# Kernel tuning notes

Hardware: AMD Instinct MI355X
Metric: run time of the kernel (lower is better)

The kernel has to match this reference:

```python
import jax, jax.numpy as jnp
from jax import lax
import numpy as np

B, L, C, H, F = 8, 512, 512, 8, 2048
NC, NA, K, W, S = 4, 6, 5, 4, 50
HD = C // H
R = 2 * W + 1
PAD = (K - 1) // 2
H2 = 2
HD2 = C // H2
VOCAB = 256
EPS = 1e-6


def ln_ch(x, g, b):
    # LayerNorm over channel dim of (B,C,L) (torch transposes to (B,L,C), norms last dim)
    m = jnp.mean(x, axis=1, keepdims=True)
    v = jnp.mean((x - m) ** 2, axis=1, keepdims=True)
    return (x - m) * lax.rsqrt(v + EPS) * g[None, :, None] + b[None, :, None]


def conv1x1(w, b, x):
    # 1x1 Conv1d == channel-mixing matmul
    return jnp.einsum('oc,bcl->bol', w, x) + b[None, :, None]


def forward_fn(tokens, style_values, mask, embed,
               cw_dw_w, cw_dw_b, cw_ln_g, cw_ln_b, cw_pw1_w, cw_pw1_b,
               cw_pw2_w, cw_pw2_b, cw_gamma,
               aq_w, aq_b, ak_w, ak_b, av_w, av_b, ao_w, ao_b,
               rel_k_emb, rel_v_emb, ln1_g, ln1_b, ln2_g, ln2_b,
               ffn_w1, ffn_b1, ffn_w2, ffn_b2,
               style_key, sq_w, sq_b, sk_w, sk_b, sv_w, sv_b, so_w, so_b,
               sn_g, sn_b):
    x = embed[tokens]                 # (B,L,C)
    x = jnp.transpose(x, (0, 2, 1))   # (B,C,L)

    # --- ConvNeXt stack ---
    for i in range(NC):
        x = x * mask
        res = x
        xp = jnp.pad(x, ((0, 0), (0, 0), (PAD, PAD)), mode='edge')  # replicate pad
        h = lax.conv_general_dilated(xp, cw_dw_w[i][:, None, :], (1,), 'VALID',
                                     feature_group_count=C,
                                     dimension_numbers=('NCH', 'OIH', 'NCH'))
        h = h + cw_dw_b[i][None, :, None]
        h = h * mask
        h = ln_ch(h, cw_ln_g[i], cw_ln_b[i])
        h = conv1x1(cw_pw1_w[i], cw_pw1_b[i], h)
        h = jax.nn.gelu(h, approximate=False)
        h = conv1x1(cw_pw2_w[i], cw_pw2_b[i], h)
        x = res + cw_gamma[i][None, :, None] * h
        x = x * mask

    # --- AttnEncoder with windowed relative-position attention ---
    x = x * mask
    attn_mask = mask[:, :, :, None] * mask[:, :, None, :]   # (B,1,L,L)
    t = jnp.arange(L)
    diff = t[None, :] - t[:, None]
    wmask = (jnp.abs(diff) <= W).astype(x.dtype)             # (L,L)
    idx = jnp.clip(diff, -W, W) + W                          # (L,L) in [0,2W]
    scale = HD ** -0.5
    for i in range(NA):
        res = x
        q = conv1x1(aq_w[i], aq_b[i], x).reshape(B, H, HD, L).transpose(0, 1, 3, 2) * scale
        k = conv1x1(ak_w[i], ak_b[i], x).reshape(B, H, HD, L).transpose(0, 1, 3, 2)
        v = conv1x1(av_w[i], av_b[i], x).reshape(B, H, HD, L).transpose(0, 1, 3, 2)
        scores = jnp.einsum('bhld,bhmd->bhlm', q, k)
        rel_k = rel_k_emb[i][idx]                             # (L,L,HD)
        scores = scores + jnp.einsum('bhld,lmd->bhlm', q, rel_k) * wmask[None, None]
        scores = jnp.where(attn_mask == 0, -10000.0, scores)
        attn = jax.nn.softmax(scores, axis=-1)
        out = jnp.einsum('bhlm,bhmd->bhld', attn, v)
        rel_v = rel_v_emb[i][idx] * wmask[:, :, None]         # (L,L,HD)
        out = out + jnp.einsum('bhlm,lmd->bhld', attn, rel_v)
        out = out.transpose(0, 1, 3, 2).reshape(B, C, L)
        out = conv1x1(ao_w[i], ao_b[i], out)
        x = ln_ch(res + out, ln1_g[i], ln1_b[i])
        h = conv1x1(ffn_w1[i], ffn_b1[i], x * mask)
        h = jax.nn.relu(h) * mask
        h = conv1x1(ffn_w2[i], ffn_b2[i], h) * mask
        x = ln_ch(x + h, ln2_g[i], ln2_b[i])
    x = x * mask

    # --- StyleAttention ---
    xt = jnp.transpose(x, (0, 2, 1))          # (B,L,C)
    mask_t = jnp.transpose(mask, (0, 2, 1))   # (B,L,1)
    sscale = C ** -0.5                         # torch uses full dim, not head_dim

    def style_layer(xin, i):
        q = (xin @ sq_w[i].T + sq_b[i]).reshape(B, L, H2, HD2)
        kk = jnp.tanh(style_key[0] @ sk_w[i].T + sk_b[i]).reshape(S, H2, HD2)
        vals = jnp.broadcast_to(style_values, (B, S, C))
        vv = (vals @ sv_w[i].T + sv_b[i]).reshape(B, S, H2, HD2)
        sc = jnp.einsum('bthd,shd->hbts', q, kk) * sscale
        a = jax.nn.softmax(sc, axis=-1)
        a = jnp.where(mask_t[None] == 0, 0.0, a)
        o = jnp.einsum('hbts,bshd->bthd', a, vv).reshape(B, L, C)
        o = o @ so_w[i].T + so_b[i]
        return o * mask_t

    out1 = style_layer(xt, 0)
    x1 = xt + out1
    out2 = style_layer(x1, 1)
    x2 = xt + out2
    m = jnp.mean(x2, axis=-1, keepdims=True)
    var = jnp.mean((x2 - m) ** 2, axis=-1, keepdims=True)
    xn = (x2 - m) * lax.rsqrt(var + EPS) * sn_g + sn_b
    x = jnp.transpose(xn, (0, 2, 1)) * mask
    return x


def setup_inputs() -> dict:
    key = jax.random.key(0)
    kit = iter(jax.random.split(key, 48))

    def rn(shape, s=0.02):
        return jax.random.normal(next(kit), shape, jnp.float32) * s

    inp = {
        'tokens': jax.random.randint(next(kit), (B, L), 0, VOCAB),
        'style_values': rn((1, S, C), 1.0),
        'mask': jnp.ones((B, 1, L), jnp.float32),
        'embed': rn((VOCAB, C), 1.0),
        'cw_dw_w': rn((NC, C, K)), 'cw_dw_b': jnp.zeros((NC, C)),
        'cw_ln_g': jnp.ones((NC, C)), 'cw_ln_b': jnp.zeros((NC, C)),
        'cw_pw1_w': rn((NC, 4 * C, C)), 'cw_pw1_b': jnp.zeros((NC, 4 * C)),
        'cw_pw2_w': rn((NC, C, 4 * C)), 'cw_pw2_b': jnp.zeros((NC, C)),
        'cw_gamma': jnp.full((NC, C), 1e-6, jnp.float32),
        'aq_w': rn((NA, C, C)), 'aq_b': jnp.zeros((NA, C)),
        'ak_w': rn((NA, C, C)), 'ak_b': jnp.zeros((NA, C)),
        'av_w': rn((NA, C, C)), 'av_b': jnp.zeros((NA, C)),
        'ao_w': rn((NA, C, C)), 'ao_b': jnp.zeros((NA, C)),
        'rel_k_emb': rn((NA, R, HD)), 'rel_v_emb': rn((NA, R, HD)),
        'ln1_g': jnp.ones((NA, C)), 'ln1_b': jnp.zeros((NA, C)),
        'ln2_g': jnp.ones((NA, C)), 'ln2_b': jnp.zeros((NA, C)),
        'ffn_w1': rn((NA, F, C)), 'ffn_b1': jnp.zeros((NA, F)),
        'ffn_w2': rn((NA, C, F)), 'ffn_b2': jnp.zeros((NA, C)),
        'style_key': rn((1, S, C)),
        'sq_w': rn((2, C, C)), 'sq_b': jnp.zeros((2, C)),
        'sk_w': rn((2, C, C)), 'sk_b': jnp.zeros((2, C)),
        'sv_w': rn((2, C, C)), 'sv_b': jnp.zeros((2, C)),
        'so_w': rn((2, C, C)), 'so_b': jnp.zeros((2, C)),
        'sn_g': jnp.ones((C,)), 'sn_b': jnp.zeros((C,)),
    }
    return inp


def reference(tokens, style_values, mask, embed,
              cw_dw_w, cw_dw_b, cw_ln_g, cw_ln_b, cw_pw1_w, cw_pw1_b,
              cw_pw2_w, cw_pw2_b, cw_gamma,
              aq_w, aq_b, ak_w, ak_b, av_w, av_b, ao_w, ao_b,
              rel_k_emb, rel_v_emb, ln1_g, ln1_b, ln2_g, ln2_b,
              ffn_w1, ffn_b1, ffn_w2, ffn_b2,
              style_key, sq_w, sq_b, sk_w, sk_b, sv_w, sv_b, so_w, so_b,
              sn_g, sn_b):
    return forward_fn(tokens, style_values, mask, embed,
                      cw_dw_w, cw_dw_b, cw_ln_g, cw_ln_b, cw_pw1_w, cw_pw1_b,
                      cw_pw2_w, cw_pw2_b, cw_gamma,
                      aq_w, aq_b, ak_w, ak_b, av_w, av_b, ao_w, ao_b,
                      rel_k_emb, rel_v_emb, ln1_g, ln1_b, ln2_g, ln2_b,
                      ffn_w1, ffn_b1, ffn_w2, ffn_b2,
                      style_key, sq_w, sq_b, sk_w, sk_b, sv_w, sv_b, so_w, so_b,
                      sn_g, sn_b)
```

## Files before the change

### kernel.cpp

```cpp
#include <hip/hip_runtime.h>
#include <cstdint>

#define Bb 8
#define Ll 512
#define Cc 512
#define Hh 8
#define HD 64
#define Ff 2048
#define Ss 50
#define NROWS 4096
#define QKVS 1536

typedef __attribute__((ext_vector_type(8))) short short8v;
typedef __attribute__((ext_vector_type(4))) float f32x4;

__device__ __forceinline__ float wave_sum(float v){
  #pragma unroll
  for (int o=32;o>=1;o>>=1) v += __shfl_xor(v,o);
  return v;
}
__device__ __forceinline__ float bf2f(unsigned short u){
  return __uint_as_float(((unsigned)u) << 16);
}

// ... 377 lines not shown
    if (s+1 < nsteps){
      int ko = (s+1) << 5;
      ah_ = *(const short8v*)(Ahg + ko);
      al_ = *(const short8v*)(Alg + ko);
      bh0_ = *(const short8v*)(Bhg + ko);
      bl0_ = *(const short8v*)(Blg + ko);
      if constexpr (NF==4){
        bh1_ = *(const short8v*)(Bhg + (size_t)64*K + ko);
        bl1_ = *(const short8v*)(Blg + (size_t)64*K + ko);
      }
      if (AMASK && am == 0.f){ ah_ ^= ah_; al_ ^= al_; }
    }
    __syncthreads();
    int fr = lane & 15, fc = (lane >> 4) << 3;
    short8v ahf[2], alf[2], bhf[NF], blf[NF];
    #pragma unroll
    for (int mt=0; mt<2; ++mt){
      int r = (wr<<5) + (mt<<4) + fr;
      ahf[mt] = *(const short8v*)&AhS[st][r][fc];
      alf[mt] = *(const short8v*)&AlS[st][r][fc];
    }
    #pragma unroll
    for (int nt=0; nt<NF; ++nt){
      int r = (NF==4 ? (wc<<6) : (wc<<5)) + (nt<<4) + fr;
      bhf[nt] = *(const short8v*)&BhS[st][r][fc];
      blf[nt] = *(const short8v*)&BlS[st][r][fc];
    }
    #pragma unroll
    for (int mt=0; mt<2; ++mt)
      #pragma unroll
      for (int nt=0; nt<NF; ++nt){
        f32x4 c = acc[mt][nt];
        c = __builtin_amdgcn_mfma_f32_16x16x32_bf16(ahf[mt], bhf[nt], c, 0,0,0);
        c = __builtin_amdgcn_mfma_f32_16x16x32_bf16(ahf[mt], blf[nt], c, 0,0,0);
        c = __builtin_amdgcn_mfma_f32_16x16x32_bf16(alf[mt], bhf[nt], c, 0,0,0);
        acc[mt][nt] = c;
      }
    if (s+1 < nsteps){
      int nb = st ^ 1;
      *(short8v*)&AhS[nb][sr][sc] = ah_;
      *(short8v*)&AlS[nb][sr][sc] = al_;
      *(short8v*)&BhS[nb][sr][sc] = bh0_;
      *(short8v*)&BlS[nb][sr][sc] = bl0_;
      if constexpr (NF==4){
        *(short8v*)&BhS[nb][sr+64][sc] = bh1_;
        *(short8v*)&BlS[nb][sr+64][sc] = bl1_;
      }
    }
    st ^= 1;
  }

  int rb = row0 + (wr<<5) + ((lane>>4)<<2);
  int cb = col0 + (NF==4 ? (wc<<6) : (wc<<5)) + (lane & 15);
  float bs[NF], gm[NF];
  int which = 0;
  if constexpr (EPI==EPI_QKV) which = blockIdx.x >> 2;
  #pragma unroll
  for (int nt=0; nt<NF; ++nt){
    int col = cb + (nt<<4);
    if constexpr (EPI==EPI_QKV){
      const float* bp = (which==0) ? bias : (which==1) ? res : gamma;
      bs[nt] = bp[col & 511];
    } else {
      bs[nt] = bias[col];
      if constexpr (EPI==EPI_RES_GAMMA_MASK) gm[nt] = gamma[col];
    }
  }
  float qscale = 1.f;
  if constexpr (EPI==EPI_QKV) qscale = (which==0) ? scale : 1.f;

  if constexpr (OUT==2){
    if (which == 2){
      #pragma unroll
      for (int mt=0; mt<2; ++mt){
        int row = rb + (mt<<4);
        int b = row >> 9, tok = row & 511;
        #pragma unroll
        for (int nt=0; nt<NF; ++nt){
          int dglob = cb + (nt<<4) - 1024;
          size_t vt = ((size_t)b*512 + dglob)*512 + tok;
          unsigned short h4[4], l4[4];
          #pragma unroll
          for (int j=0; j<4; ++j)
            splitc(acc[mt][nt][j] + bs[nt], h4[j], l4[j]);
          *(ushort4*)&VTh[vt] = make_ushort4(h4[0],h4[1],h4[2],h4[3]);
          *(ushort4*)&VTl[vt] = make_ushort4(l4[0],l4[1],l4[2],l4[3]);
        }
      }
      return;
    }
    #pragma unroll
    for (int mt=0; mt<2; ++mt)
      #pragma unroll
      for (int j=0; j<4; ++j){
        int row = rb + (mt<<4) + j;
        #pragma unroll
        for (int nt=0; nt<NF; ++nt){
          float v = (acc[mt][nt][j] + bs[nt]) * qscale;
          size_t oidx = (size_t)row*O + cb + (nt<<4);
          unsigned short h,l; splitc(v,h,l); Yh[oidx]=h; Yl[oidx]=l;
        }
      }
    return;
  }

  #pragma unroll
  for (int mt=0; mt<2; ++mt)
    #pragma unroll
    for (int j=0; j<4; ++j){
      int row = rb + (mt<<4) + j;
      float rm = 1.f;
      if constexpr (EPI==EPI_RELU_MASK || EPI==EPI_RES_MASK || EPI==EPI_RES_GAMMA_MASK)
        rm = rowmask[row];
      const float* rr = nullptr;
      if constexpr (EPI==EPI_RES || EPI==EPI_RES_MASK || EPI==EPI_RES_GAMMA_MASK)
        rr = res + (size_t)row*O + cb;
      #pragma unroll
      for (int nt=0; nt<NF; ++nt){
        float v = acc[mt][nt][j] + bs[nt];
        if constexpr (EPI==EPI_SCALE) v *= scale;
        else if constexpr (EPI==EPI_QKV) v *= qscale;
        else if constexpr (EPI==EPI_GELU) v = 0.5f*v*(1.f+erff(v*0.7071067811865475f));
        else if constexpr (EPI==EPI_RES) v = rr[nt<<4] + v;
        else if constexpr (EPI==EPI_RELU_MASK) v = fmaxf(v,0.f)*rm;
        else if constexpr (EPI==EPI_RES_MASK) v = rr[nt<<4] + v*rm;
        else if constexpr (EPI==EPI_RES_GAMMA_MASK) v = (rr[nt<<4] + gm[nt]*v)*rm;
        size_t oidx = (size_t)row*O + cb + (nt<<4);
        if constexpr (OUT==0) Y[oidx] = v;
        else if constexpr (OUT==3){
          Y[oidx] = v;
          unsigned short h,l; splitc(v,h,l); Yh[oidx]=h; Yl[oidx]=l;
        }
        else { unsigned short h,l; splitc(v,h,l); Yh[oidx]=h; Yl[oidx]=l; }
      }
    }
}

template<int EPI, bool AMASK, int OUT>
__global__ __launch_bounds__(256) void gemm_big(
    const unsigned short* __restrict__ Ah, const unsigned short* __restrict__ Al,
    const unsigned short* __restrict__ Wh, const unsigned short* __restrict__ Wl,
    const float* __restrict__ bias, const float* __restrict__ res,
    const float* __restrict__ gamma, const float* __restrict__ rowmask,
    float* __restrict__ Y, unsigned short* __restrict__ Yh,
    unsigned short* __restrict__ Yl, unsigned short* __restrict__ VTh,
    unsigned short* __restrict__ VTl, int K, int O, float scale)
{
  __shared__ unsigned short AhS[128][40], AlS[128][40];
  __shared__ unsigned short BhS[128][40], BlS[128][40];
  int t = threadIdx.x;
  int row0 = blockIdx.y << 7, col0 = blockIdx.x << 7;
  int lane = t & 63, wid = t >> 6;
  int wr = wid >> 1, wc = wid & 1;

  int sr = t >> 2, sc = (t & 3) << 3;
  const unsigned short* Ahg = Ah + (size_t)(row0 + sr)*K + sc;
  const unsigned short* Alg = Al + (size_t)(row0 + sr)*K + sc;
  const unsigned short* Bhg = Wh + (size_t)(col0 + sr)*K + sc;
  const unsigned short* Blg = Wl + (size_t)(col0 + sr)*K + sc;
  bool az0 = false, az1 = false;
  if (AMASK){ az0 = (rowmask[row0+sr] == 0.f); az1 = (rowmask[row0+sr+64] == 0.f); }

  f32x4 acc[4][4] = {};
  int nsteps = K >> 5;
  short8v a0h,a0l,a1h,a1l,b0h,b0l,b1h,b1l;
  a0h = *(const short8v*)(Ahg);
  a0l = *(const short8v*)(Alg);
  a1h = *(const short8v*)(Ahg + (size_t)64*K);
  a1l = *(const short8v*)(Alg + (size_t)64*K);
  b0h = *(const short8v*)(Bhg);
  b0l = *(const short8v*)(Blg);
  b1h = *(const short8v*)(Bhg + (size_t)64*K);
  b1l = *(const short8v*)(Blg + (size_t)64*K);

  for (int s = 0; s < nsteps; ++s){
    if (AMASK){
      if (az0){ a0h ^= a0h; a0l ^= a0l; }
      if (az1){ a1h ^= a1h; a1l ^= a1l; }
    }
    __syncthreads();
    *(short8v*)&AhS[sr][sc] = a0h;    *(short8v*)&AlS[sr][sc] = a0l;
    *(short8v*)&AhS[sr+64][sc] = a1h; *(short8v*)&AlS[sr+64][sc] = a1l;
    *(short8v*)&BhS[sr][sc] = b0h;    *(short8v*)&BlS[sr][sc] = b0l;
    *(short8v*)&BhS[sr+64][sc] = b1h; *(short8v*)&BlS[sr+64][sc] = b1l;
    __syncthreads();
    if (s+1 < nsteps){
      int ko = (s+1) << 5;
      a0h = *(const short8v*)(Ahg + ko);
      a0l = *(const short8v*)(Alg + ko);
      a1h = *(const short8v*)(Ahg + (size_t)64*K + ko);
      a1l = *(const short8v*)(Alg + (size_t)64*K + ko);
      b0h = *(const short8v*)(Bhg + ko);
      b0l = *(const short8v*)(Blg + ko);
      b1h = *(const short8v*)(Bhg + (size_t)64*K + ko);
      b1l = *(const short8v*)(Blg + (size_t)64*K + ko);
    }
    int fr = lane & 15, fc = (lane >> 4) << 3;
    short8v ahf[4], alf[4], bhf[4], blf[4];
    #pragma unroll
    for (int mt=0; mt<4; ++mt){
      int r = (wr<<6) + (mt<<4) + fr;
      ahf[mt] = *(const short8v*)&AhS[r][fc];
      alf[mt] = *(const short8v*)&AlS[r][fc];
    }
    #pragma unroll
    for (int nt=0; nt<4; ++nt){
      int r = (wc<<6) + (nt<<4) + fr;
      bhf[nt] = *(const short8v*)&BhS[r][fc];
      blf[nt] = *(const short8v*)&BlS[r][fc];
    }
    #pragma unroll
    for (int mt=0; mt<4; ++mt)
      #pragma unroll
      for (int nt=0; nt<4; ++nt){
        f32x4 c = acc[mt][nt];
        c = __builtin_amdgcn_mfma_f32_16x16x32_bf16(ahf[mt], bhf[nt], c, 0,0,0);
        c = __builtin_amdgcn_mfma_f32_16x16x32_bf16(ahf[mt], blf[nt], c, 0,0,0);
        c = __builtin_amdgcn_mfma_f32_16x16x32_bf16(alf[mt], bhf[nt], c, 0,0,0);
        acc[mt][nt] = c;
      }
  }

  int rb = row0 + (wr<<6) + ((lane>>4)<<2);
  int cb = col0 + (wc<<6) + (lane & 15);
  float bs[4];
  int which = 0;
  if constexpr (EPI==EPI_QKV) which = blockIdx.x >> 2;
  #pragma unroll
  for (int nt=0; nt<4; ++nt){
    int col = cb + (nt<<4);
    if constexpr (EPI==EPI_QKV){
      const float* bp = (which==0) ? bias : (which==1) ? res : gamma;
      bs[nt] = bp[col & 511];
    } else {
      bs[nt] = bias[col];
    }
  }
  float qscale = 1.f;
  if constexpr (EPI==EPI_QKV) qscale = (which==0) ? scale : 1.f;

  if constexpr (OUT==2){
    if (which == 2){
      #pragma unroll
      for (int mt=0; mt<4; ++mt){
        int row = rb + (mt<<4);
        int b = row >> 9, tok = row & 511;
        #pragma unroll
        for (int nt=0; nt<4; ++nt){
          int dglob = cb + (nt<<4) - 1024;
          size_t vt = ((size_t)b*512 + dglob)*512 + tok;
          unsigned short h4[4], l4[4];
          #pragma unroll
          for (int j=0; j<4; ++j)
            splitc(acc[mt][nt][j] + bs[nt], h4[j], l4[j]);
          *(ushort4*)&VTh[vt] = make_ushort4(h4[0],h4[1],h4[2],h4[3]);
          *(ushort4*)&VTl[vt] = make_ushort4(l4[0],l4[1],l4[2],l4[3]);
        }
      }
      return;
    }
    #pragma unroll
    for (int mt=0; mt<4; ++mt)
      #pragma unroll
      for (int j=0; j<4; ++j){
        int row = rb + (mt<<4) + j;
        #pragma unroll
        for (int nt=0; nt<4; ++nt){
          float v = (acc[mt][nt][j] + bs[nt]) * qscale;
          size_t oidx = (size_t)row*O + cb + (nt<<4);
          unsigned short h,l; splitc(v,h,l); Yh[oidx]=h; Yl[oidx]=l;
        }
      }
    return;
  }

  #pragma unroll
  for (int mt=0; mt<4; ++mt)
    #pragma unroll
    for (int j=0; j<4; ++j){
      int row = rb + (mt<<4) + j;
      float rm = 1.f;
      if constexpr (EPI==EPI_RELU_MASK) rm = rowmask[row];
      #pragma unroll
      for (int nt=0; nt<4; ++nt){
        float v = acc[mt][nt][j] + bs[nt];
        if constexpr (EPI==EPI_GELU) v = 0.5f*v*(1.f+erff(v*0.7071067811865475f));
        else if constexpr (EPI==EPI_RELU_MASK) v = fmaxf(v,0.f)*rm;
        size_t oidx = (size_t)row*O + cb + (nt<<4);
        if constexpr (OUT==0) Y[oidx] = v;
        else { unsigned short h,l; splitc(v,h,l); Yh[oidx]=h; Yl[oidx]=l; }
      }
    }
}

__global__ __launch_bounds__(256) void attn_mf(
    const unsigned short* __restrict__ Ph_g, const unsigned short* __restrict__ Pl_g,
    const unsigned short* __restrict__ VTh_g, const unsigned short* __restrict__ VTl_g,
    const float* __restrict__ relk, const float* __restrict__ relv,
    const float* __restrict__ mask, unsigned short* __restrict__ Oh,
    unsigned short* __restrict__ Ol)
{
  __shared__ float ms_[512];
  __shared__ float rv[9][64];
  __shared__ float qrel[16][16];
  __shared__ float red1[4][16];
  __shared__ float red2[4][16];
  __shared__ __align__(16) unsigned short Spool[16*520];
  unsigned short (*Qh)[72]  = (unsigned short(*)[72])(Spool);
  unsigned short (*Ql)[72]  = (unsigned short(*)[72])(Spool + 1152);
  unsigned short (*Rkh)[72] = (unsigned short(*)[72])(Spool + 2304);
  unsigned short (*Rkl)[72] = (unsigned short(*)[72])(Spool + 3456);
  unsigned short (*Sp)[520] = (unsigned short(*)[520])(Spool);

  int id = blockIdx.x;
  int xcd = id & 7, kk = id >> 3;
  int bh_ = xcd*8 + (kk >> 5);
  int qt = kk & 31;
  int h = bh_ & 7, b_ = bh_ >> 3;
  int t = threadIdx.x;
  int l0 = qt * 16;
  const size_t rowoff = (size_t)b_ * 512;
  int lane = t & 63, w = t >> 6;

  ms_[t] = mask[rowoff + t]; ms_[t+256] = mask[rowoff + t + 256];
  for (int i = t; i < 576; i += 256) ((float*)rv)[i] = relv[i];
  {
    int r = t >> 4, c = (t & 15) << 2;
    float4 v;
    if (r < 9) v = *(const float4*)&relk[r*64 + c];
    else { v.x=0.f; v.y=0.f; v.z=0.f; v.w=0.f; }
    split4(v, &Rkh[r][c], &Rkl[r][c]);
  }
  {
    int idx = t & 127; int r = idx >> 3, c = (idx & 7) << 3;
    size_t g = (rowoff + l0 + r)*QKVS + h*64 + c;
    if (t < 128) *(short8v*)&Qh[r][c] = *(const short8v*)&Ph_g[g];
    else         *(short8v*)&Ql[r][c] = *(const short8v*)&Pl_g[g];
  }
  __syncthreads();

  int fr = lane & 15, fc = (lane >> 4) << 3;
  int qbase = (lane>>4) << 2;
  short8v ah0 = *(const short8v*)&Qh[fr][fc];
  short8v ah1 = *(const short8v*)&Qh[fr][32+fc];
  short8v al0 = *(const short8v*)&Ql[fr][fc];
  short8v al1 = *(const short8v*)&Ql[fr][32+fc];

  if (w == 0){
    short8v rh0 = *(const short8v*)&Rkh[fr][fc];
    short8v rh1 = *(const short8v*)&Rkh[fr][32+fc];
    short8v rl0 = *(const short8v*)&Rkl[fr][fc];
    short8v rl1 = *(const short8v*)&Rkl[fr][32+fc];
    f32x4 c4 = {};
    c4 = __builtin_amdgcn_mfma_f32_16x16x32_bf16(ah0,rh0,c4,0,0,0);
    c4 = __builtin_amdgcn_mfma_f32_16x16x32_bf16(ah1,rh1,c4,0,0,0);
    c4 = __builtin_amdgcn_mfma_f32_16x16x32_bf16(ah0,rl0,c4,0,0,0);
    c4 = __builtin_amdgcn_mfma_f32_16x16x32_bf16(ah1,rl1,c4,0,0,0);
    c4 = __builtin_amdgcn_mfma_f32_16x16x32_bf16(al0,rh0,c4,0,0,0);
    c4 = __builtin_amdgcn_mfma_f32_16x16x32_bf16(al1,rh1,c4,0,0,0);
    #pragma unroll
    for (int j = 0; j < 4; ++j) qrel[qbase + j][fr] = c4[j];
  }
  __syncthreads();

  f32x4 sreg[8];
  #pragma unroll
  for (int tt = 0; tt < 8; ++tt){
    int br = tt*64 + w*16 + fr;
    const unsigned short* krh = Ph_g + (rowoff + br)*QKVS + 512 + h*64;
    const unsigned short* krl = Pl_g + (rowoff + br)*QKVS + 512 + h*64;
    short8v bh0 = *(const short8v*)(krh + fc);
    short8v bh1 = *(const short8v*)(krh + 32 + fc);
    short8v bl0 = *(const short8v*)(krl + fc);
    short8v bl1 = *(const short8v*)(krl + 32 + fc);
    f32x4 c4 = {};
    c4 = __builtin_amdgcn_mfma_f32_16x16x32_bf16(ah0,bh0,c4,0,0,0);
    c4 = __builtin_amdgcn_mfma_f32_16x16x32_bf16(ah1,bh1,c4,0,0,0);
    c4 = __builtin_amdgcn_mfma_f32_16x16x32_bf16(ah0,bl0,c4,0,0,0);
    c4 = __builtin_amdgcn_mfma_f32_16x16x32_bf16(ah1,bl1,c4,0,0,0);
    c4 = __builtin_amdgcn_mfma_f32_16x16x32_bf16(al0,bh0,c4,0,0,0);
    c4 = __builtin_amdgcn_mfma_f32_16x16x32_bf16(al1,bh1,c4,0,0,0);
    int m = tt*64 + w*16 + fr;
    float mm_ = ms_[m];
    #pragma unroll
    for (int j = 0; j < 4; ++j){
      int q = qbase + j;
      int l = l0 + q;
      float s = c4[j];
      int dlt = m - l + 4;
      if (dlt >= 0 && dlt <= 8) s += qrel[q][dlt];
      if (ms_[l] * mm_ == 0.f) s = -10000.f;
      c4[j] = s;
    }
    sreg[tt] = c4;
  }

  float mx[4], sm[4], inv[4];
  #pragma unroll
  for (int j = 0; j < 4; ++j){
    float v = sreg[0][j];
    #pragma unroll
    for (int tt = 1; tt < 8; ++tt) v = fmaxf(v, sreg[tt][j]);
    #pragma unroll
    for (int o = 8; o >= 1; o >>= 1) v = fmaxf(v, __shfl_xor(v, o));
    mx[j] = v;
  }
  if (fr == 0){
    #pragma unroll
    for (int j = 0; j < 4; ++j) red1[w][qbase + j] = mx[j];
  }
  __syncthreads();
  #pragma unroll
  for (int j = 0; j < 4; ++j){
    int q = qbase + j;
    mx[j] = fmaxf(fmaxf(red1[0][q], red1[1][q]), fmaxf(red1[2][q], red1[3][q]));
  }
  #pragma unroll
  for (int j = 0; j < 4; ++j) sm[j] = 0.f;
  #pragma unroll
  for (int tt = 0; tt < 8; ++tt){
    f32x4 c4 = sreg[tt];
    #pragma unroll
    for (int j = 0; j < 4; ++j){
      float e = expf(c4[j] - mx[j]);
      c4[j] = e;
      sm[j] += e;
    }
    sreg[tt] = c4;
  }
  #pragma unroll
  for (int j = 0; j < 4; ++j){
    float v = sm[j];
    #pragma unroll
    for (int o = 8; o >= 1; o >>= 1) v += __shfl_xor(v, o);
    sm[j] = v;
  }
  if (fr == 0){
    #pragma unroll
    for (int j = 0; j < 4; ++j) red2[w][qbase + j] = sm[j];
  }
  #pragma unroll
  for (int tt = 0; tt < 8; ++tt){
    int m = tt*64 + w*16 + fr;
    #pragma unroll
    for (int j = 0; j < 4; ++j)
      Sp[qbase + j][m] = f2bf_rne(sreg[tt][j]);
  }
  __syncthreads();
  #pragma unroll
  for (int j = 0; j < 4; ++j){
    int q = qbase + j;
    inv[j] = 1.f / (red2[0][q] + red2[1][q] + red2[2][q] + red2[3][q]);
  }

  f32x4 oacc = {};
  const unsigned short* vrh = VTh_g + ((size_t)b_*512 + h*64 + w*16 + fr)*512;
  const unsigned short* vrl = VTl_g + ((size_t)b_*512 + h*64 + w*16 + fr)*512;
  #pragma unroll
  for (int tt = 0; tt < 8; ++tt){
    #pragma unroll
    for (int ks = 0; ks < 2; ++ks){
      int moff = tt*64 + ks*32 + fc;
      short8v ap = *(const short8v*)&Sp[fr][moff];
      short8v bh = *(const short8v*)(vrh + moff);
      short8v bl = *(const short8v*)(vrl + moff);
      oacc = __builtin_amdgcn_mfma_f32_16x16x32_bf16(ap,bh,oacc,0,0,0);
      oacc = __builtin_amdgcn_mfma_f32_16x16x32_bf16(ap,bl,oacc,0,0,0);
    }
  }
  {
    int d = w*16 + fr;
    #pragma unroll
    for (int j = 0; j < 4; ++j){
      int q = qbase + j;
      int l = l0 + q;
      float val = oacc[j];
      #pragma unroll
      for (int dlt = 0; dlt < 9; ++dlt){
        int m = l + dlt - 4;
        if (m >= 0 && m < 512){
          float e = bf2f(Sp[q][m]);
          val += e * rv[dlt][d];
        }
      }
      val *= inv[j];
      unsigned short hh, ll_; splitc(val, hh, ll_);
      size_t oidx = ((rowoff + l) << 9) + h*64 + d;
      Oh[oidx] = hh; Ol[oidx] = ll_;
    }
  }
}

__global__ __launch_bounds__(256) void transpose_out_k(const float* __restrict__ xn,
    const float* __restrict__ mask, float* __restrict__ out){
  __shared__ float tile[32][33];
  int b_ = blockIdx.z; int c0 = blockIdx.x*32; int l0 = blockIdx.y*32;
  int tx = threadIdx.x & 31, ty = threadIdx.x >> 5;
  #pragma unroll
  for (int r=0;r<4;r++){
    int l = l0 + ty + r*8;
    tile[ty + r*8][tx] = xn[(((size_t)(b_*512 + l))<<9) + c0 + tx];
  }
  __syncthreads();
  float mm = mask[b_*512 + l0 + tx];
  #pragma unroll
  for (int r=0;r<4;r++){
    int c = c0 + ty + r*8;
    out[(((size_t)(b_*512 + c))<<9) + l0 + tx] = tile[tx][ty + r*8] * mm;
  }
}

extern "C" void kernel_launch(void* const* d_in, const int* in_sizes, int n_in,
                              void* d_out, int out_size, void* d_ws, size_t ws_size,
                              hipStream_t stream) {
  const int*   tokens   = (const int*)  d_in[0];
  const float* style_v  = (const float*)d_in[1];
  const float* mask     = (const float*)d_in[2];
  const float* embed_w  = (const float*)d_in[3];
  const float* cw_dw_w  = (const float*)d_in[4];
  const float* cw_dw_b  = (const float*)d_in[5];
  const float* cw_ln_g  = (const float*)d_in[6];
  const float* cw_ln_b  = (const float*)d_in[7];
  const float* cw_pw1_w = (const float*)d_in[8];
  const float* cw_pw1_b = (const float*)d_in[9];
  const float* cw_pw2_w = (const float*)d_in[10];
  const float* cw_pw2_b = (const float*)d_in[11];
  const float* cw_gamma = (const float*)d_in[12];
  const float* aq_w = (const float*)d_in[13];
  const float* aq_b = (const float*)d_in[14];
  const float* ak_w = (const float*)d_in[15];
  const float* ak_b = (const float*)d_in[16];
  const float* av_w = (const float*)d_in[17];
  const float* av_b = (const float*)d_in[18];
  const float* ao_w = (const float*)d_in[19];
  const float* ao_b = (const float*)d_in[20];
  const float* rel_k = (const float*)d_in[21];
  const float* rel_v = (const float*)d_in[22];
  const float* ln1_g = (const float*)d_in[23];
  const float* ln1_b = (const float*)d_in[24];
  const float* ln2_g = (const float*)d_in[25];
  const float* ln2_b = (const float*)d_in[26];
  const float* ffn_w1 = (const float*)d_in[27];
  const float* ffn_b1 = (const float*)d_in[28];
  const float* ffn_w2 = (const float*)d_in[29];
  const float* ffn_b2 = (const float*)d_in[30];
  const float* style_key = (const float*)d_in[31];
  const float* sq_w = (const float*)d_in[32];
  const float* sq_b = (const float*)d_in[33];
  const float* sk_w = (const float*)d_in[34];
  const float* sk_b = (const float*)d_in[35];
  const float* sv_w = (const float*)d_in[36];
  const float* sv_b = (const float*)d_in[37];
  const float* so_w = (const float*)d_in[38];
  const float* so_b = (const float*)d_in[39];
  const float* sn_g = (const float*)d_in[40];
  const float* sn_b = (const float*)d_in[41];

  const int N = NROWS;
  char* cur = (char*)d_ws;
  auto nextF = [&](size_t n)->float*{ float* p=(float*)cur; cur += n*sizeof(float); return p; };
  auto nextU = [&](size_t n)->unsigned short*{ unsigned short* p=(unsigned short*)cur; cur += n*2; return p; };

  float* X   = nextF((size_t)N*512);
  float* T   = nextF((size_t)N*512);
  float* Qb  = nextF((size_t)N*512);
  float* Vb  = nextF((size_t)N*512);
  unsigned short* Xh = nextU((size_t)N*512);
  unsigned short* Xl = nextU((size_t)N*512);
  unsigned short* Th = nextU((size_t)N*512);
  unsigned short* Tl = nextU((size_t)N*512);
  unsigned short* Hbh = nextU((size_t)N*2048);
  unsigned short* Hbl = nextU((size_t)N*2048);
  unsigned short* QKVh = nextU((size_t)N*QKVS);
  unsigned short* QKVl = nextU((size_t)N*QKVS);
  unsigned short* VTh = nextU((size_t)8*512*512);
  unsigned short* VTl = nextU((size_t)8*512*512);
  unsigned short* pw1h = nextU(4194304); unsigned short* pw1l = nextU(4194304);
  unsigned short* pw2h = nextU(4194304); unsigned short* pw2l = nextU(4194304);
  unsigned short* qkvh = nextU((size_t)6*QKVS*512); unsigned short* qkvl = nextU((size_t)6*QKVS*512);
  unsigned short* aoh  = nextU(1572864); unsigned short* aol  = nextU(1572864);
  unsigned short* f1h  = nextU(6291456); unsigned short* f1l  = nextU(6291456);
  unsigned short* f2h  = nextU(6291456); unsigned short* f2l  = nextU(6291456);
  unsigned short* sqh  = nextU(524288);  unsigned short* sql  = nextU(524288);
  unsigned short* soh  = nextU(524288);  unsigned short* sol  = nextU(524288);
  unsigned short* KKsh = nextU(65536); unsigned short* KKsl = nextU(65536);
  unsigned short* VTsh = nextU(65536); unsigned short* VTsl = nextU(65536);

  split_all<<<dim3(512,8),256,0,stream>>>(cw_pw1_w, cw_pw2_w, ao_w, ffn_w1,
      ffn_w2, sq_w, so_w, aq_w, ak_w, av_w,
      pw1h, pw1l, pw2h, pw2l, aoh, aol, f1h, f1l, f2h, f2l,
      sqh, sql, soh, sol, qkvh, qkvl);

  dim3 gm512(8,64), gbig2048(16,32), gbigqkv(12,32);

  embed_k<<<4096,128,0,stream>>>(tokens, embed_w, mask, X);

  for (int i=0;i<4;i++){
    dwln_k<<<4096,128,0,stream>>>(X, cw_dw_w + (size_t)i*512*5, cw_dw_b + i*512,
        mask, cw_ln_g+i*512, cw_ln_b+i*512, Th, Tl);
    gemm_big<EPI_GELU,false,1><<<gbig2048,256,0,stream>>>(Th, Tl,
        pw1h + (size_t)i*1048576, pw1l + (size_t)i*1048576,
        cw_pw1_b+i*2048, nullptr, nullptr, nullptr, nullptr, Hbh, Hbl,
        nullptr, nullptr, 512, 2048, 0.f);
    if (i < 3)
      gemm_ps<EPI_RES_GAMMA_MASK,false,0,2><<<gm512,256,0,stream>>>(Hbh, Hbl,
          pw2h + (size_t)i*1048576, pw2l + (size_t)i*1048576,
          cw_pw2_b+i*512, X, cw_gamma+i*512, mask, X, nullptr, nullptr,
          nullptr, nullptr, 2048, 512, 0.f);
    else
      gemm_ps<EPI_RES_GAMMA_MASK,false,3,2><<<gm512,256,0,stream>>>(Hbh, Hbl,
          pw2h + (size_t)i*1048576, pw2l + (size_t)i*1048576,
          cw_pw2_b+i*512, X, cw_gamma+i*512, mask, X, Xh, Xl,
          nullptr, nullptr, 2048, 512, 0.f);
  }

  for (int i=0;i<6;i++){
    gemm_big<EPI_QKV,false,2><<<gbigqkv,256,0,stream>>>(Xh, Xl,
        qkvh + (size_t)i*QKVS*512, qkvl + (size_t)i*QKVS*512,
        aq_b+i*512, ak_b+i*512, av_b+i*512, nullptr, nullptr, QKVh, QKVl,
        VTh, VTl, 512, QKVS, 0.125f);
    attn_mf<<<2048,256,0,stream>>>(QKVh, QKVl, VTh, VTl,
        rel_k + (size_t)i*9*64, rel_v + (size_t)i*9*64, mask, Th, Tl);
    gemm_ps<EPI_RES,false,0,2><<<gm512,256,0,stream>>>(Th, Tl,
        aoh + (size_t)i*262144, aol + (size_t)i*262144,
        ao_b+i*512, X, nullptr, nullptr, Qb, nullptr, nullptr,
        nullptr, nullptr, 512, 512, 0.f);
    ln_rows<true,false><<<1024,256,0,stream>>>(Qb, ln1_g+i*512, ln1_b+i*512,
        nullptr, X, Xh, Xl, N);
    gemm_big<EPI_RELU_MASK,true,1><<<gbig2048,256,0,stream>>>(Xh, Xl,
        f1h + (size_t)i*1048576, f1l + (size_t)i*1048576,
        ffn_b1+i*2048, nullptr, nullptr, mask, nullptr, Hbh, Hbl,
        nullptr, nullptr, 512, 2048, 0.f);
    gemm_ps<EPI_RES_MASK,false,0,2><<<gm512,256,0,stream>>>(Hbh, Hbl,
        f2h + (size_t)i*1048576, f2l + (size_t)i*1048576,
        ffn_b2+i*512, X, nullptr, mask, Qb, nullptr, nullptr,
        nullptr, nullptr, 2048, 512, 0.f);
    if (i < 5)
      ln_rows<true,false><<<1024,256,0,stream>>>(Qb, ln2_g+i*512, ln2_b+i*512,
          nullptr, X, Xh, Xl, N);
    else
      ln_rows<true,true><<<1024,256,0,stream>>>(Qb, ln2_g+i*512, ln2_b+i*512,
          mask, X, Xh, Xl, N);
  }

  style_prep<<<dim3(8,4),256,0,stream>>>(style_key, style_v, sk_w, sk_b,
      sv_w, sv_b, KKsh, KKsl, VTsh, VTsl);

  gemm_ps<EPI_BIAS,false,1,2><<<gm512,256,0,stream>>>(Xh, Xl, sqh, sql,
      sq_b, nullptr, nullptr, nullptr, nullptr, QKVh, QKVl,
      nullptr, nullptr, 512, 512, 0.f);
  style_mf<<<256,256,0,stream>>>(QKVh, QKVl, KKsh, KKsl, VTsh, VTsl,
      mask, Th, Tl);
  gemm_ps<EPI_RES_MASK,false,1,2><<<gm512,256,0,stream>>>(Th, Tl, soh, sol,
      so_b, X, nullptr, mask, nullptr, Hbh, Hbl,
      nullptr, nullptr, 512, 512, 0.f);
  gemm_ps<EPI_BIAS,false,1,2><<<gm512,256,0,stream>>>(Hbh, Hbl, sqh+262144, sql+262144,
      sq_b+512, nullptr, nullptr, nullptr, nullptr, QKVh, QKVl,
      nullptr, nullptr, 512, 512, 0.f);
  style_mf<<<256,256,0,stream>>>(QKVh, QKVl, KKsh+32768, KKsl+32768,
      VTsh+32768, VTsl+32768, mask, Th, Tl);
  gemm_ps<EPI_RES_MASK,false,0,2><<<gm512,256,0,stream>>>(Th, Tl, soh+262144, sol+262144,
      so_b+512, X, nullptr, mask, Vb, nullptr, nullptr,
      nullptr, nullptr, 512, 512, 0.f);

  ln_rows<false,false><<<1024,256,0,stream>>>(Vb, sn_g, sn_b, nullptr,
      Qb, nullptr, nullptr, N);
  transpose_out_k<<<dim3(16,16,8),256,0,stream>>>(Qb, mask, (float*)d_out);
}
```

Measured before the change: 1.804 ms.

## Process 32 query rows per attention block to reuse K and V loads

The attention kernel now handles two 16-row query tiles per block, so each wave's K and V fragments loaded from global memory feed two MFMA accumulators instead of one. The grid shrinks from 2048 to 1024 blocks and the shared-memory buffers double in size. This halves the redundant K/V global traffic per query. In exchange it raises register pressure (two sets of score registers) and LDS use, which may lower occupancy.

```diff
diff --git a/kernel.cpp b/kernel.cpp
--- a/kernel.cpp
+++ b/kernel.cpp
@@ -703,23 +703,23 @@
 {
   __shared__ float ms_[512];
   __shared__ float rv[9][64];
-  __shared__ float qrel[16][16];
-  __shared__ float red1[4][16];
-  __shared__ float red2[4][16];
-  __shared__ __align__(16) unsigned short Spool[16*520];
+  __shared__ float qrel[32][16];
+  __shared__ float red1[4][32];
+  __shared__ float red2[4][32];
+  __shared__ __align__(16) unsigned short Spool[32*520];
   unsigned short (*Qh)[72]  = (unsigned short(*)[72])(Spool);
-  unsigned short (*Ql)[72]  = (unsigned short(*)[72])(Spool + 1152);
-  unsigned short (*Rkh)[72] = (unsigned short(*)[72])(Spool + 2304);
-  unsigned short (*Rkl)[72] = (unsigned short(*)[72])(Spool + 3456);
+  unsigned short (*Ql)[72]  = (unsigned short(*)[72])(Spool + 2304);
+  unsigned short (*Rkh)[72] = (unsigned short(*)[72])(Spool + 4608);
+  unsigned short (*Rkl)[72] = (unsigned short(*)[72])(Spool + 5760);
   unsigned short (*Sp)[520] = (unsigned short(*)[520])(Spool);
 
   int id = blockIdx.x;
   int xcd = id & 7, kk = id >> 3;
-  int bh_ = xcd*8 + (kk >> 5);
-  int qt = kk & 31;
+  int bh_ = xcd*8 + (kk >> 4);
+  int qt = kk & 15;
   int h = bh_ & 7, b_ = bh_ >> 3;
   int t = threadIdx.x;
-  int l0 = qt * 16;
+  int l0 = qt * 32;
   const size_t rowoff = (size_t)b_ * 512;
   int lane = t & 63, w = t >> 6;
 
@@ -732,39 +732,47 @@
     else { v.x=0.f; v.y=0.f; v.z=0.f; v.w=0.f; }
     split4(v, &Rkh[r][c], &Rkl[r][c]);
   }
-  {
-    int idx = t & 127; int r = idx >> 3, c = (idx & 7) << 3;
+  for (int i = t; i < 512; i += 256){
+    int r = (i & 255) >> 3, c = (i & 7) << 3;
     size_t g = (rowoff + l0 + r)*QKVS + h*64 + c;
-    if (t < 128) *(short8v*)&Qh[r][c] = *(const short8v*)&Ph_g[g];
+    if (i < 256) *(short8v*)&Qh[r][c] = *(const short8v*)&Ph_g[g];
     else         *(short8v*)&Ql[r][c] = *(const short8v*)&Pl_g[g];
   }
   __syncthreads();
 
   int fr = lane & 15, fc = (lane >> 4) << 3;
   int qbase = (lane>>4) << 2;
-  short8v ah0 = *(const short8v*)&Qh[fr][fc];
-  short8v ah1 = *(const short8v*)&Qh[fr][32+fc];
-  short8v al0 = *(const short8v*)&Ql[fr][fc];
-  short8v al1 = *(const short8v*)&Ql[fr][32+fc];
-
-  if (w == 0){
+  short8v a0h0 = *(const short8v*)&Qh[fr][fc];
+  short8v a0h1 = *(const short8v*)&Qh[fr][32+fc];
+  short8v a0l0 = *(const short8v*)&Ql[fr][fc];
+  short8v a0l1 = *(const short8v*)&Ql[fr][32+fc];
+  short8v a1h0 = *(const short8v*)&Qh[16+fr][fc];
+  short8v a1h1 = *(const short8v*)&Qh[16+fr][32+fc];
+  short8v a1l0 = *(const short8v*)&Ql[16+fr][fc];
+  short8v a1l1 = *(const short8v*)&Ql[16+fr][32+fc];
+
+  if (w < 2){
     short8v rh0 = *(const short8v*)&Rkh[fr][fc];
     short8v rh1 = *(const short8v*)&Rkh[fr][32+fc];
     short8v rl0 = *(const short8v*)&Rkl[fr][fc];
     short8v rl1 = *(const short8v*)&Rkl[fr][32+fc];
+    short8v qa0 = (w==0) ? a0h0 : a1h0;
+    short8v qa1 = (w==0) ? a0h1 : a1h1;
+    short8v qb0 = (w==0) ? a0l0 : a1l0;
+    short8v qb1 = (w==0) ? a0l1 : a1l1;
     f32x4 c4 = {};
-    c4 = __builtin_amdgcn_mfma_f32_16x16x32_bf16(ah0,rh0,c4,0,0,0);
-    c4 = __builtin_amdgcn_mfma_f32_16x16x32_bf16(ah1,rh1,c4,0,0,0);
-    c4 = __builtin_amdgcn_mfma_f32_16x16x32_bf16(ah0,rl0,c4,0,0,0);
-    c4 = __builtin_amdgcn_mfma_f32_16x16x32_bf16(ah1,rl1,c4,0,0,0);
-    c4 = __builtin_amdgcn_mfma_f32_16x16x32_bf16(al0,rh0,c4,0,0,0);
-    c4 = __builtin_amdgcn_mfma_f32_16x16x32_bf16(al1,rh1,c4,0,0,0);
-    #pragma unroll
-    for (int j = 0; j < 4; ++j) qrel[qbase + j][fr] = c4[j];
+    c4 = __builtin_amdgcn_mfma_f32_16x16x32_bf16(qa0,rh0,c4,0,0,0);
+    c4 = __builtin_amdgcn_mfma_f32_16x16x32_bf16(qa1,rh1,c4,0,0,0);
+    c4 = __builtin_amdgcn_mfma_f32_16x16x32_bf16(qa0,rl0,c4,0,0,0);
+    c4 = __builtin_amdgcn_mfma_f32_16x16x32_bf16(qa1,rl1,c4,0,0,0);
+    c4 = __builtin_amdgcn_mfma_f32_16x16x32_bf16(qb0,rh0,c4,0,0,0);
+    c4 = __builtin_amdgcn_mfma_f32_16x16x32_bf16(qb1,rh1,c4,0,0,0);
+    #pragma unroll
+    for (int j = 0; j < 4; ++j) qrel[w*16 + qbase + j][fr] = c4[j];
   }
   __syncthreads();
 
-  f32x4 sreg[8];
+  f32x4 sreg0[8], sreg1[8];
   #pragma unroll
   for (int tt = 0; tt < 8; ++tt){
     int br = tt*64 + w*16 + fr;
@@ -774,87 +782,123 @@
     short8v bh1 = *(const short8v*)(krh + 32 + fc);
     short8v bl0 = *(const short8v*)(krl + fc);
     short8v bl1 = *(const short8v*)(krl + 32 + fc);
-    f32x4 c4 = {};
-    c4 = __builtin_amdgcn_mfma_f32_16x16x32_bf16(ah0,bh0,c4,0,0,0);
-    c4 = __builtin_amdgcn_mfma_f32_16x16x32_bf16(ah1,bh1,c4,0,0,0);
-    c4 = __builtin_amdgcn_mfma_f32_16x16x32_bf16(ah0,bl0,c4,0,0,0);
-    c4 = __builtin_amdgcn_mfma_f32_16x16x32_bf16(ah1,bl1,c4,0,0,0);
-    c4 = __builtin_amdgcn_mfma_f32_16x16x32_bf16(al0,bh0,c4,0,0,0);
-    c4 = __builtin_amdgcn_mfma_f32_16x16x32_bf16(al1,bh1,c4,0,0,0);
+    f32x4 c0 = {}, c1 = {};
+    c0 = __builtin_amdgcn_mfma_f32_16x16x32_bf16(a0h0,bh0,c0,0,0,0);
+    c1 = __builtin_amdgcn_mfma_f32_16x16x32_bf16(a1h0,bh0,c1,0,0,0);
+    c0 = __builtin_amdgcn_mfma_f32_16x16x32_bf16(a0h1,bh1,c0,0,0,0);
+    c1 = __builtin_amdgcn_mfma_f32_16x16x32_bf16(a1h1,bh1,c1,0,0,0);
+    c0 = __builtin_amdgcn_mfma_f32_16x16x32_bf16(a0h0,bl0,c0,0,0,0);
+    c1 = __builtin_amdgcn_mfma_f32_16x16x32_bf16(a1h0,bl0,c1,0,0,0);
+    c0 = __builtin_amdgcn_mfma_f32_16x16x32_bf16(a0h1,bl1,c0,0,0,0);
+    c1 = __builtin_amdgcn_mfma_f32_16x16x32_bf16(a1h1,bl1,c1,0,0,0);
+    c0 = __builtin_amdgcn_mfma_f32_16x16x32_bf16(a0l0,bh0,c0,0,0,0);
+    c1 = __builtin_amdgcn_mfma_f32_16x16x32_bf16(a1l0,bh0,c1,0,0,0);
+    c0 = __builtin_amdgcn_mfma_f32_16x16x32_bf16(a0l1,bh1,c0,0,0,0);
+    c1 = __builtin_amdgcn_mfma_f32_16x16x32_bf16(a1l1,bh1,c1,0,0,0);
     int m = tt*64 + w*16 + fr;
     float mm_ = ms_[m];
     #pragma unroll
     for (int j = 0; j < 4; ++j){
       int q = qbase + j;
-      int l = l0 + q;
-      float s = c4[j];
-      int dlt = m - l + 4;
-      if (dlt >= 0 && dlt <= 8) s += qrel[q][dlt];
-      if (ms_[l] * mm_ == 0.f) s = -10000.f;
-      c4[j] = s;
-    }
-    sreg[tt] = c4;
-  }
-
-  float mx[4], sm[4], inv[4];
+      {
+        int l = l0 + q;
+        float s = c0[j];
+        int dlt = m - l + 4;
+        if (dlt >= 0 && dlt <= 8) s += qrel[q][dlt];
+        if (ms_[l] * mm_ == 0.f) s = -10000.f;
+        c0[j] = s;
+      }
+      {
+        int l = l0 + 16 + q;
+        float s = c1[j];
+        int dlt = m - l + 4;
+        if (dlt >= 0 && dlt <= 8) s += qrel[16 + q][dlt];
+        if (ms_[l] * mm_ == 0.f) s = -10000.f;
+        c1[j] = s;
+      }
+    }
+    sreg0[tt] = c0; sreg1[tt] = c1;
+  }
+
+  float mx0[4], mx1[4], sm0[4], sm1[4], inv0[4], inv1[4];
   #pragma unroll
   for (int j = 0; j < 4; ++j){
-    float v = sreg[0][j];
-    #pragma unroll
-    for (int tt = 1; tt < 8; ++tt) v = fmaxf(v, sreg[tt][j]);
-    #pragma unroll
-    for (int o = 8; o >= 1; o >>= 1) v = fmaxf(v, __shfl_xor(v, o));
-    mx[j] = v;
+    float v0 = sreg0[0][j], v1 = sreg1[0][j];
+    #pragma unroll
+    for (int tt = 1; tt < 8; ++tt){
+      v0 = fmaxf(v0, sreg0[tt][j]);
+      v1 = fmaxf(v1, sreg1[tt][j]);
+    }
+    #pragma unroll
+    for (int o = 8; o >= 1; o >>= 1){
+      v0 = fmaxf(v0, __shfl_xor(v0, o));
+      v1 = fmaxf(v1, __shfl_xor(v1, o));
+    }
+    mx0[j] = v0; mx1[j] = v1;
   }
   if (fr == 0){
     #pragma unroll
-    for (int j = 0; j < 4; ++j) red1[w][qbase + j] = mx[j];
+    for (int j = 0; j < 4; ++j){
+      red1[w][qbase + j] = mx0[j];
+      red1[w][16 + qbase + j] = mx1[j];
+    }
   }
   __syncthreads();
   #pragma unroll
   for (int j = 0; j < 4; ++j){
     int q = qbase + j;
-    mx[j] = fmaxf(fmaxf(red1[0][q], red1[1][q]), fmaxf(red1[2][q], red1[3][q]));
-  }
-  #pragma unroll
-  for (int j = 0; j < 4; ++j) sm[j] = 0.f;
+    mx0[j] = fmaxf(fmaxf(red1[0][q], red1[1][q]), fmaxf(red1[2][q], red1[3][q]));
+    mx1[j] = fmaxf(fmaxf(red1[0][16+q], red1[1][16+q]), fmaxf(red1[2][16+q], red1[3][16+q]));
+  }
+  #pragma unroll
+  for (int j = 0; j < 4; ++j){ sm0[j] = 0.f; sm1[j] = 0.f; }
   #pragma unroll
   for (int tt = 0; tt < 8; ++tt){
-    f32x4 c4 = sreg[tt];
+    f32x4 c0 = sreg0[tt], c1 = sreg1[tt];
     #pragma unroll
     for (int j = 0; j < 4; ++j){
-      float e = expf(c4[j] - mx[j]);
-      c4[j] = e;
-      sm[j] += e;
-    }
-    sreg[tt] = c4;
+      float e0 = expf(c0[j] - mx0[j]);
+      float e1 = expf(c1[j] - mx1[j]);
+      c0[j] = e0; c1[j] = e1;
+      sm0[j] += e0; sm1[j] += e1;
+    }
+    sreg0[tt] = c0; sreg1[tt] = c1;
   }
   #pragma unroll
   for (int j = 0; j < 4; ++j){
-    float v = sm[j];
-    #pragma unroll
-    for (int o = 8; o >= 1; o >>= 1) v += __shfl_xor(v, o);
-    sm[j] = v;
+    float v0 = sm0[j], v1 = sm1[j];
+    #pragma unroll
+    for (int o = 8; o >= 1; o >>= 1){
+      v0 += __shfl_xor(v0, o);
+      v1 += __shfl_xor(v1, o);
+    }
+    sm0[j] = v0; sm1[j] = v1;
   }
   if (fr == 0){
     #pragma unroll
-    for (int j = 0; j < 4; ++j) red2[w][qbase + j] = sm[j];
+    for (int j = 0; j < 4; ++j){
+      red2[w][qbase + j] = sm0[j];
+      red2[w][16 + qbase + j] = sm1[j];
+    }
   }
   #pragma unroll
   for (int tt = 0; tt < 8; ++tt){
     int m = tt*64 + w*16 + fr;
     #pragma unroll
-    for (int j = 0; j < 4; ++j)
-      Sp[qbase + j][m] = f2bf_rne(sreg[tt][j]);
+    for (int j = 0; j < 4; ++j){
+      Sp[qbase + j][m]      = f2bf_rne(sreg0[tt][j]);
+      Sp[16 + qbase + j][m] = f2bf_rne(sreg1[tt][j]);
+    }
   }
   __syncthreads();
   #pragma unroll
   for (int j = 0; j < 4; ++j){
     int q = qbase + j;
-    inv[j] = 1.f / (red2[0][q] + red2[1][q] + red2[2][q] + red2[3][q]);
-  }
-
-  f32x4 oacc = {};
+    inv0[j] = 1.f / (red2[0][q] + red2[1][q] + red2[2][q] + red2[3][q]);
+    inv1[j] = 1.f / (red2[0][16+q] + red2[1][16+q] + red2[2][16+q] + red2[3][16+q]);
+  }
+
+  f32x4 oacc0 = {}, oacc1 = {};
   const unsigned short* vrh = VTh_g + ((size_t)b_*512 + h*64 + w*16 + fr)*512;
   const unsigned short* vrl = VTl_g + ((size_t)b_*512 + h*64 + w*16 + fr)*512;
   #pragma unroll
@@ -862,32 +906,54 @@
     #pragma unroll
     for (int ks = 0; ks < 2; ++ks){
       int moff = tt*64 + ks*32 + fc;
-      short8v ap = *(const short8v*)&Sp[fr][moff];
+      short8v ap0 = *(const short8v*)&Sp[fr][moff];
+      short8v ap1 = *(const short8v*)&Sp[16+fr][moff];
       short8v bh = *(const short8v*)(vrh + moff);
       short8v bl = *(const short8v*)(vrl + moff);
-      oacc = __builtin_amdgcn_mfma_f32_16x16x32_bf16(ap,bh,oacc,0,0,0);
-      oacc = __builtin_amdgcn_mfma_f32_16x16x32_bf16(ap,bl,oacc,0,0,0);
+      oacc0 = __builtin_amdgcn_mfma_f32_16x16x32_bf16(ap0,bh,oacc0,0,0,0);
+      oacc1 = __builtin_amdgcn_mfma_f32_16x16x32_bf16(ap1,bh,oacc1,0,0,0);
+      oacc0 = __builtin_amdgcn_mfma_f32_16x16x32_bf16(ap0,bl,oacc0,0,0,0);
+      oacc1 = __builtin_amdgcn_mfma_f32_16x16x32_bf16(ap1,bl,oacc1,0,0,0);
     }
   }
   {
     int d = w*16 + fr;
     #pragma unroll
     for (int j = 0; j < 4; ++j){
-      int q = qbase + j;
-      int l = l0 + q;
-      float val = oacc[j];
-      #pragma unroll
-      for (int dlt = 0; dlt < 9; ++dlt){
-        int m = l + dlt - 4;
-        if (m >= 0 && m < 512){
-          float e = bf2f(Sp[q][m]);
-          val += e * rv[dlt][d];
+      {
+        int q = qbase + j;
+        int l = l0 + q;
+        float val = oacc0[j];
+        #pragma unroll
+        for (int dlt = 0; dlt < 9; ++dlt){
+          int m = l + dlt - 4;
+          if (m >= 0 && m < 512){
+            float e = bf2f(Sp[q][m]);
+            val += e * rv[dlt][d];
+          }
         }
-      }
-      val *= inv[j];
-      unsigned short hh, ll_; splitc(val, hh, ll_);
-      size_t oidx = ((rowoff + l) << 9) + h*64 + d;
-      Oh[oidx] = hh; Ol[oidx] = ll_;
+        val *= inv0[j];
+        unsigned short hh, ll_; splitc(val, hh, ll_);
+        size_t oidx = ((rowoff + l) << 9) + h*64 + d;
+        Oh[oidx] = hh; Ol[oidx] = ll_;
+      }
+      {
+        int q = 16 + qbase + j;
+        int l = l0 + q;
+        float val = oacc1[j];
+        #pragma unroll
+        for (int dlt = 0; dlt < 9; ++dlt){
+          int m = l + dlt - 4;
+          if (m >= 0 && m < 512){
+            float e = bf2f(Sp[q][m]);
+            val += e * rv[dlt][d];
+          }
+        }
+        val *= inv1[j];
+        unsigned short hh, ll_; splitc(val, hh, ll_);
+        size_t oidx = ((rowoff + l) << 9) + h*64 + d;
+        Oh[oidx] = hh; Ol[oidx] = ll_;
+      }
     }
   }
 }
@@ -1020,7 +1086,7 @@
         qkvh + (size_t)i*QKVS*512, qkvl + (size_t)i*QKVS*512,
         aq_b+i*512, ak_b+i*512, av_b+i*512, nullptr, nullptr, QKVh, QKVl,
         VTh, VTl, 512, QKVS, 0.125f);
-    attn_mf<<<2048,256,0,stream>>>(QKVh, QKVl, VTh, VTl,
+    attn_mf<<<1024,256,0,stream>>>(QKVh, QKVl, VTh, VTl,
         rel_k + (size_t)i*9*64, rel_v + (size_t)i*9*64, mask, Th, Tl);
     gemm_ps<EPI_RES,false,0,2><<<gm512,256,0,stream>>>(Th, Tl,
         aoh + (size_t)i*262144, aol + (size_t)i*262144,
```

New measurement: 1.720 ms, median of 2. -4.6%, faster.
